# Kernel optimization log

Measured on AMD Instinct MI355X. Metric: run time of the kernel, lower is better.

## Reference

```python
import jax, jax.numpy as jnp
import numpy as np

# HashGrid config (from tcnn encoding config)
N_LEVELS = 16
N_FEATS = 2
LOG2_T = 19
T = 1 << LOG2_T  # 524288 entries per level
BASE_RES = 16
PER_LEVEL_SCALE = 1.5
PRIMES = (1, 2654435761, 805459861)  # tcnn spatial hash primes

# MLP config
N_NEURONS = 128
N_HIDDEN = 8  # 8 hidden layers -> w_in + 7 hidden matmuls + w_out
ENC_DIM = N_LEVELS * N_FEATS + 4  # 32 hashgrid feats + 4 identity dims
OUT_DIM = 3


def _level_params(level):
    # tcnn: scale = exp2(level*log2(s)) * base_res - 1 ; res = ceil(scale)+1
    scale = 2.0 ** (level * np.log2(PER_LEVEL_SCALE)) * BASE_RES - 1.0
    res = int(np.ceil(scale)) + 1
    return float(scale), res


def hash_grid_encode(x3, tables):
    """x3: [N,3] in [0,1]; tables: [L,T,F] -> [N, L*F]."""
    offs = jnp.array([[(c >> d) & 1 for d in range(3)] for c in range(8)], jnp.int32)  # [8,3]
    feats = []
    for l in range(N_LEVELS):
        scale, res = _level_params(l)
        pos = x3 * scale + 0.5
        p0 = jnp.floor(pos)
        frac = pos - p0                      # [N,3]
        p0 = p0.astype(jnp.int32)
        coords = p0[:, None, :] + offs[None, :, :]  # [N,8,3]
        # trilinear weights per corner
        w = jnp.where(offs[None, :, :] == 1, frac[:, None, :], 1.0 - frac[:, None, :]).prod(-1)  # [N,8]
        if res ** 3 <= T:
            # dense indexing (tcnn uses strided index while stride <= hashmap_size)
            idx = (coords[..., 0] + coords[..., 1] * res + coords[..., 2] * res * res) % T
        else:
            c = coords.astype(jnp.uint32)
            h = (c[..., 0] * jnp.uint32(PRIMES[0])
                 ^ c[..., 1] * jnp.uint32(PRIMES[1])
                 ^ c[..., 2] * jnp.uint32(PRIMES[2]))
            idx = (h & jnp.uint32(T - 1)).astype(jnp.int32)
        g = tables[l][idx]                   # [N,8,F] gather
        feats.append(jnp.einsum('nc,ncf->nf', w, g))  # [N,F]
    return jnp.concatenate(feats, axis=-1)   # [N,32]


def setup_inputs() -> dict:
    key = jax.random.key(0)
    kx, kt, k0, kh, ko = jax.random.split(key, 5)
    N = 524288
    x = jax.random.uniform(kx, (N, 16), dtype=jnp.float32)
    # tcnn hash tables init ~ U(-1e-4, 1e-4)
    tables = jax.random.uniform(kt, (N_LEVELS, T, N_FEATS), dtype=jnp.float32,
                                minval=-1e-4, maxval=1e-4)
    w_in = jax.random.normal(k0, (ENC_DIM, N_NEURONS), dtype=jnp.float32) * (1.0 / np.sqrt(ENC_DIM))
    w_hidden = jax.random.normal(kh, (N_HIDDEN - 1, N_NEURONS, N_NEURONS), dtype=jnp.float32) * (1.0 / np.sqrt(N_NEURONS))
    w_out = jax.random.normal(ko, (N_NEURONS, OUT_DIM), dtype=jnp.float32) * (1.0 / np.sqrt(N_NEURONS))
    return {"x": x, "tables": tables, "w_in": w_in, "w_hidden": w_hidden, "w_out": w_out}


def reference(x, tables, w_in, w_hidden, w_out):
    enc = jnp.concatenate([hash_grid_encode(x[:, :3], tables), x[:, 3:7]], axis=-1)  # [N,36]
    h = jax.nn.relu(enc @ w_in)
    for i in range(w_hidden.shape[0]):  # static small loop over 7 hidden layers
        h = jax.nn.relu(h @ w_hidden[i])
    return h @ w_out  # [N,3], linear output activation
```

## Files before the change

### kernel.cpp

```cpp
#include <hip/hip_runtime.h>
#include <math.h>

#define NPTS 524288
#define TSZ  524288
#define TMASK (TSZ - 1)

typedef _Float16 half8  __attribute__((ext_vector_type(8)));
typedef _Float16 half4v __attribute__((ext_vector_type(4)));
typedef float    f32x4  __attribute__((ext_vector_type(4)));

#define QSCALE    1.27e6f
#define ENC_SCALE 1024.f
#define DECF      (1e-4f / 127.f * ENC_SCALE)
#define WIN_SCALE (1.f / ENC_SCALE)

struct LevelParams {
  float    scale[16];
  int      res[16];
  unsigned dense_mask;
};

#define OFF_TAB 262144
#define OFF_XYZ 17039360
#define OFF_XID 25427968
#define OFF_ENC 29622272

__device__ __forceinline__ void convert_w_elem(int i,
    const float* __restrict__ w_in, const float* __restrict__ w_hidden,
    const float* __restrict__ w_out, _Float16* __restrict__ dst)
{
  float v;
  int dstidx;
  if (i < 8192) {
    int n = i >> 6, k = i & 63;
    if (k < 32) {
      int p = k >> 3, jj = (k >> 1) & 3, f = k & 1;
      int lev = (jj == 0) ? p : (4 + 3 * p + (jj - 1));
      v = w_in[(2 * lev + f) * 128 + n] * WIN_SCALE;
    } else if (k < 36) {
      v = w_in[k * 128 + n];
    } else v = 0.f;
    dstidx = n * 64 + (k ^ ((n & 7) << 3));
  } else if (i < 122880) {
    int r = i - 8192;
    int j = r >> 14, t = r & 16383;
    int n = t >> 7, k = t & 127;
    int q = ((k & 7) << 4) | (k >> 3);
    v = w_hidden[(j * 128 + q) * 128 + n];
    int h = k >> 6;
    dstidx = 8192 + j * 16384 + h * 8192 + n * 64 + ((k & 63) ^ ((n & 7) << 3));
  } else {
    int t = i - 122880;
    int n = t >> 7, k = t & 127;
    int q = ((k & 7) << 4) | (k >> 3);
    v = (n < 3) ? w_out[q * 3 + n] : 0.f;
    int h = k >> 6;
    dstidx = 122880 + h * 1024 + n * 64 + ((k & 63) ^ ((n & 7) << 3));
  }
  dst[dstidx] = (_Float16)v;
}

__global__ __launch_bounds__(256, 4)
void prep(const float* __restrict__ tables, const float* __restrict__ x,
          const float* __restrict__ w_in, const float* __restrict__ w_hidden,
          const float* __restrict__ w_out,
          unsigned* __restrict__ tab8w, f32x4* __restrict__ xyz,
          _Float16* __restrict__ xid, _Float16* __restrict__ wts)
{
  int i = blockIdx.x * 256 + threadIdx.x;
  if (i < 4194304) {
    f32x4 v = ((const f32x4*)tables)[i];
    int q0 = (int)rintf(v[0] * QSCALE);
    int q1 = (int)rintf(v[1] * QSCALE);
    int q2 = (int)rintf(v[2] * QSCALE);
    int q3 = (int)rintf(v[3] * QSCALE);
    tab8w[i] = (unsigned)(q0 & 255) | ((unsigned)(q1 & 255) << 8) |
               ((unsigned)(q2 & 255) << 16) | ((unsigned)(q3 & 255) << 24);
  } else if (i < 4718592) {
    int p = i - 4194304;
    f32x4 a = ((const f32x4*)x)[(size_t)p * 4];
    f32x4 b = ((const f32x4*)x)[(size_t)p * 4 + 1];
    xyz[p] = a;
    half4v h = {(_Float16)a[3], (_Float16)b[0], (_Float16)b[1], (_Float16)b[2]};
    *(half4v*)(xid + (size_t)p * 4) = h;
  } else {
    convert_w_elem(i - 4718592, w_in, w_hidden, w_out, wts);
  }
}

template<bool DENSE>
__device__ __forceinline__ void enc_one(float x0, float x1, float x2, float s,
    int res, unsigned rr, const unsigned short* __restrict__ tb,
    float& f0, float& f1)
{
  const float px = x0 * s + 0.5f, py = x1 * s + 0.5f, pz = x2 * s + 0.5f;
  const float fx = floorf(px), fy = floorf(py), fz = floorf(pz);
  const float wx1 = px - fx, wy1 = py - fy, wz1 = pz - fz;
  const float wx0 = 1.f - wx1, wy0 = 1.f - wy1, wz0 = 1.f - wz1;
  const unsigned ix = (unsigned)(int)fx, iy = (unsigned)(int)fy,
                 iz = (unsigned)(int)fz;
  unsigned t0, t1, u0, u1, v0, v1;
  if (DENSE) {
    t0 = ix; t1 = ix + 1u;
    u0 = iy * (unsigned)res; u1 = u0 + (unsigned)res;
    v0 = iz * rr; v1 = v0 + rr;
  } else {
    t0 = ix;               t1 = ix + 1u;
    u0 = iy * 2654435761u; u1 = (iy + 1u) * 2654435761u;
    v0 = iz * 805459861u;  v1 = (iz + 1u) * 805459861u;
  }
  f0 = 0.f; f1 = 0.f;
#pragma unroll
  for (int c = 0; c < 8; ++c) {
    const unsigned a = (c & 1) ? t1 : t0;
    const unsigned b = (c & 2) ? u1 : u0;
    const unsigned d = (c & 4) ? v1 : v0;
    const unsigned idx = DENSE ? (a + b + d) : ((a ^ b ^ d) & TMASK);
    const float w = ((c & 1) ? wx1 : wx0) * ((c & 2) ? wy1 : wy0) *
                    ((c & 4) ? wz1 : wz0);
    const unsigned g = tb[idx];
    f0 += w * (float)(int)(signed char)(g & 0xFFu);
    f1 += w * (float)(int)(signed char)(g >> 8);
  }
}

__global__ __launch_bounds__(256, 4)
void nrc_encode(const f32x4* __restrict__ xyz,
                const unsigned short* __restrict__ tab8,
                f32x4* __restrict__ enc16, LevelParams lp)
{
  const int bid = blockIdx.x;
  const int xcd = bid & 7;
  const int pr  = xcd >> 1;
  const int chunk = ((bid >> 3) << 1) | (xcd & 1);
  const float s0_ = lp.scale[pr];
  const int   res = lp.res[pr];
  const unsigned rr = (unsigned)(res * res);
  const float s1_ = lp.scale[4 + 3 * pr];
  const float s2_ = lp.scale[5 + 3 * pr];
  const float s3_ = lp.scale[6 + 3 * pr];
  const unsigned short* tb0 = tab8 + (size_t)pr * TSZ;
  const unsigned short* tb1 = tab8 + (size_t)(4 + 3 * pr) * TSZ;
  const unsigned short* tb2 = tab8 + (size_t)(5 + 3 * pr) * TSZ;
  const unsigned short* tb3 = tab8 + (size_t)(6 + 3 * pr) * TSZ;
  const int p0 = chunk * 1024 + threadIdx.x;

#pragma unroll 2
  for (int it = 0; it < 4; ++it) {
    const int pt = p0 + it * 256;
    const f32x4 xv = __builtin_nontemporal_load(xyz + pt);
    float f0, f1;
    half8 o;
    enc_one<true >(xv[0], xv[1], xv[2], s0_, res, rr, tb0, f0, f1);
    o[0] = (_Float16)(f0 * DECF); o[1] = (_Float16)(f1 * DECF);
    enc_one<false>(xv[0], xv[1], xv[2], s1_, 0, 0u, tb1, f0, f1);
    o[2] = (_Float16)(f0 * DECF); o[3] = (_Float16)(f1 * DECF);
    enc_one<false>(xv[0], xv[1], xv[2], s2_, 0, 0u, tb2, f0, f1);
    o[4] = (_Float16)(f0 * DECF); o[5] = (_Float16)(f1 * DECF);
    enc_one<false>(xv[0], xv[1], xv[2], s3_, 0, 0u, tb3, f0, f1);
    o[6] = (_Float16)(f0 * DECF); o[7] = (_Float16)(f1 * DECF);
    __builtin_nontemporal_store(*(const f32x4*)&o, enc16 + (size_t)pr * NPTS + pt);
  }
}

__device__ __forceinline__ void gload16(const void* g, void* l)
{
  __builtin_amdgcn_global_load_lds(
      (const __attribute__((address_space(1))) void*)g,
      (__attribute__((address_space(3))) void*)l, 16, 0, 0);
}

#define MFMA16 __builtin_amdgcn_mfma_f32_16x16x32_f16

#define STAGE(dst, srcoff, nch)                                   \
  for (int c = wave; c < (nch); c += 4)                           \
    gload16(wb + (srcoff) + c * 1024 + lane * 16, (dst) + c * 1024);

#define LOAD_A(hb)                                                \
  _Pragma("unroll")                                               \
  for (int t = 0; t < 4; ++t) {                                   \
    const char* At = A0 + t * 4096;                               \
    a0[t] = *(const half8*)(At + (((hb) + kg * 16) ^ s0));        \
    a1[t] = *(const half8*)(At + (((hb) + 64 + kg * 16) ^ s0));   \
  }

#define COMP_FRESH(WH)                                            \
  _Pragma("unroll")                                               \
  for (int n = 0; n < 8; ++n) {                                   \
    const int nr = n * 16 + c0;                                   \
    const char* Wr = (WH) + nr * 128;                             \
    const int wz = (nr & 7) << 4;                                 \
    half8 b0 = *(const half8*)(Wr + ((kg * 16) ^ wz));            \
    half8 b1 = *(const half8*)(Wr + ((64 + kg * 16) ^ wz));       \
    _Pragma("unroll")                                             \
    for (int t = 0; t < 4; ++t) {                                 \
      f32x4 z = {0.f, 0.f, 0.f, 0.f};                             \
      z = MFMA16(a0[t], b0, z, 0, 0, 0);                          \
      acc[t][n] = MFMA16(a1[t], b1, z, 0, 0, 0);                  \
    }                                                             \
  }

#define COMP_ACC(WH)                                              \
  _Pragma("unroll")                                               \
  for (int n = 0; n < 8; ++n) {                                   \
    const int nr = n * 16 + c0;                                   \
    const char* Wr = (WH) + nr * 128;                             \
    const int wz = (nr & 7) << 4;                                 \
    half8 b0 = *(const half8*)(Wr + ((kg * 16) ^ wz));            \
    half8 b1 = *(const half8*)(Wr + ((64 + kg * 16) ^ wz));       \
    _Pragma("unroll")                                             \
    for (int t = 0; t < 4; ++t) {                                 \
      acc[t][n] = MFMA16(a0[t], b0, acc[t][n], 0, 0, 0);          \
      acc[t][n] = MFMA16(a1[t], b1, acc[t][n], 0, 0, 0);          \
    }                                                             \
  }

#define RELU_WB                                                   \
  _Pragma("unroll")                                               \
  for (int t = 0; t < 4; ++t) {                                   \
    _Pragma("unroll")                                             \
    for (int r = 0; r < 4; ++r) {                                 \
      half8 v;                                                    \
      _Pragma("unroll")                                           \
      for (int n = 0; n < 8; ++n)                                 \
        v[n] = (_Float16)fmaxf(acc[t][n][r], 0.f);                \
      const int rw = dr0 + t * 16 + r;                            \
      *(half8*)(Xb + rw * 256 + ((c0 * 16) ^ ((rw & 7) << 4))) = v; \
    }                                                             \
  }

__global__ __launch_bounds__(256, 2)
void nrc_mlp(const f32x4* __restrict__ enc16, const _Float16* __restrict__ xid,
             const _Float16* __restrict__ wts, float* __restrict__ out)
{
  __shared__ __align__(16) char smem[98304];
  char* Xb  = smem;
  char* WH0 = smem + 65536;
  char* WH1 = smem + 81920;
  const char* wb = (const char*)wts;

  const int tid  = threadIdx.x;
  const int wave = tid >> 6;
  const int lane = tid & 63;
  const int blk  = blockIdx.x;

  STAGE(WH0, 0, 16);

  {
    const int gp = blk * 256 + tid;
    const int swz = (tid & 7) << 4;
    char* Xrow = Xb + tid * 256;
#pragma unroll
    for (int p = 0; p < 4; ++p) {
      f32x4 ef = enc16[(size_t)p * NPTS + gp];
      *(half8*)(Xrow + ((p * 16) ^ swz)) = *(half8*)&ef;
    }
    half8 z8;
#pragma unroll
    for (int i = 0; i < 8; ++i) z8[i] = (_Float16)0.f;
    const half4v iv = *(const half4v*)(xid + (size_t)gp * 4);
    half8 idv = z8;
    idv[0] = iv.x; idv[1] = iv.y; idv[2] = iv.z; idv[3] = iv.w;
    *(half8*)(Xrow + (64 ^ swz)) = idv;
    *(half8*)(Xrow + (80 ^ swz)) = z8;
    *(half8*)(Xrow + (96 ^ swz)) = z8;
    *(half8*)(Xrow + (112 ^ swz)) = z8;
  }
  __syncthreads();

  const int c0 = lane & 15;
  const int kg = lane >> 4;
  const int r0 = wave * 64 + c0;
  const int s0 = (r0 & 7) << 4;
  const char* A0 = Xb + (size_t)r0 * 256;
  const int dr0 = wave * 64 + kg * 4;

  f32x4 acc[4][8];
  half8 a0[4], a1[4];

  {
    STAGE(WH1, 16384, 16);
    LOAD_A(0);
    COMP_FRESH(WH0);
    RELU_WB;
  }
  __syncthreads();

#pragma unroll
  for (int j = 1; j <= 7; ++j) {
    {
      STAGE(WH0, 16384 + (j - 1) * 32768 + 16384, 16);
      LOAD_A(0);
      COMP_FRESH(WH1);
    }
    __syncthreads();
    {
      if (j < 7) {
        STAGE(WH1, 16384 + j * 32768, 16);
      } else {
        STAGE(WH1, 245760, 2);
      }
      LOAD_A(128);
      COMP_ACC(WH0);
      RELU_WB;
    }
    __syncthreads();
  }

  f32x4 zz[4];
  {
    STAGE(WH0, 247808, 2);
    LOAD_A(0);
    const char* Wr = WH1 + c0 * 128;
    const int wz = (c0 & 7) << 4;
    half8 b0 = *(const half8*)(Wr + ((kg * 16) ^ wz));
    half8 b1 = *(const half8*)(Wr + ((64 + kg * 16) ^ wz));
#pragma unroll
    for (int t = 0; t < 4; ++t) {
      f32x4 z = {0.f, 0.f, 0.f, 0.f};
      z = MFMA16(a0[t], b0, z, 0, 0, 0);
      zz[t] = MFMA16(a1[t], b1, z, 0, 0, 0);
    }
  }
  __syncthreads();
  {
    LOAD_A(128);
    const char* Wr = WH0 + c0 * 128;
    const int wz = (c0 & 7) << 4;
    half8 b0 = *(const half8*)(Wr + ((kg * 16) ^ wz));
    half8 b1 = *(const half8*)(Wr + ((64 + kg * 16) ^ wz));
#pragma unroll
    for (int t = 0; t < 4; ++t) {
      zz[t] = MFMA16(a0[t], b0, zz[t], 0, 0, 0);
      zz[t] = MFMA16(a1[t], b1, zz[t], 0, 0, 0);
    }
    if (c0 < 3) {
#pragma unroll
      for (int t = 0; t < 4; ++t) {
        const int pr0 = blk * 256 + dr0 + t * 16;
#pragma unroll
        for (int r = 0; r < 4; ++r)
          out[(size_t)(pr0 + r) * 3 + c0] = zz[t][r];
      }
    }
  }
}

extern "C" void kernel_launch(void* const* d_in, const int* in_sizes, int n_in,
                              void* d_out, int out_size, void* d_ws, size_t ws_size,
                              hipStream_t stream)
{
  const float* x        = (const float*)d_in[0];
  const float* tables   = (const float*)d_in[1];
  const float* w_in     = (const float*)d_in[2];
  const float* w_hidden = (const float*)d_in[3];
  const float* w_out    = (const float*)d_in[4];
  float* out = (float*)d_out;

  LevelParams lp;
  unsigned dm = 0;
  for (int l = 0; l < 16; ++l) {
    double scale = pow(2.0, (double)l * log2(1.5)) * 16.0 - 1.0;
    int res = (int)ceil(scale) + 1;
    lp.scale[l] = (float)scale;
    lp.res[l]   = res;
    if ((long long)res * res * res <= (long long)TSZ) dm |= (1u << l);
  }
  lp.dense_mask = dm;

  char* ws = (char*)d_ws;
  _Float16* wts   = (_Float16*)ws;
  unsigned* tab8w = (unsigned*)(ws + OFF_TAB);
  f32x4*    xyz   = (f32x4*)(ws + OFF_XYZ);
  _Float16* xid   = (_Float16*)(ws + OFF_XID);
  f32x4*    enc16 = (f32x4*)(ws + OFF_ENC);

  prep<<<18920, 256, 0, stream>>>(tables, x, w_in, w_hidden, w_out,
                                  tab8w, xyz, xid, wts);
  nrc_encode<<<2048, 256, 0, stream>>>(xyz, (const unsigned short*)tab8w,
                                       enc16, lp);
  nrc_mlp<<<2048, 256, 0, stream>>>(enc16, xid, wts, out);
}
```

Measured before the change: 533.3 us.

## Load MLP weights directly in MFMA fragment layout and batch hash-grid gathers

The weight prep now writes the fp16 weights pre-arranged in MFMA B-fragment order. This lets the MLP kernel read B operands straight from global memory, per lane, instead of staging them through LDS with block-wide barriers. Each wave now owns a private 16KB activation slice, so all __syncthreads are gone and LDS per block shrinks. The encode kernel computes all 32 gather indices before issuing the loads, which exposes more memory-level parallelism, and it halves points per block while doubling the grid. The cost is repeated global/L2 weight reads by every wave, plus higher register pressure in the encoder.

New measurement: 432.5 us. 1.23x faster.

```diff
diff --git a/kernel.cpp b/kernel.cpp
--- a/kernel.cpp
+++ b/kernel.cpp
@@ -25,39 +25,44 @@
 #define OFF_XID 25427968
 #define OFF_ENC 29622272
 
-__device__ __forceinline__ void convert_w_elem(int i,
+__device__ __forceinline__ _Float16 convert_w_val(int i,
     const float* __restrict__ w_in, const float* __restrict__ w_hidden,
-    const float* __restrict__ w_out, _Float16* __restrict__ dst)
-{
-  float v;
-  int dstidx;
+    const float* __restrict__ w_out)
+{
   if (i < 8192) {
-    int n = i >> 6, k = i & 63;
+    int b = i >> 9, r = i & 511;
+    int nt = b >> 1, s = b & 1;
+    int lane = r >> 3, e = r & 7;
+    int n = nt * 16 + (lane & 15);
+    int k = s * 32 + (lane >> 4) * 8 + e;
+    float v;
     if (k < 32) {
       int p = k >> 3, jj = (k >> 1) & 3, f = k & 1;
-      int lev = (jj == 0) ? p : (4 + 3 * p + (jj - 1));
+      int lev = jj ? (4 + 3 * p + jj - 1) : p;
       v = w_in[(2 * lev + f) * 128 + n] * WIN_SCALE;
     } else if (k < 36) {
       v = w_in[k * 128 + n];
     } else v = 0.f;
-    dstidx = n * 64 + (k ^ ((n & 7) << 3));
+    return (_Float16)v;
   } else if (i < 122880) {
-    int r = i - 8192;
-    int j = r >> 14, t = r & 16383;
-    int n = t >> 7, k = t & 127;
+    int t = i - 8192;
+    int j = t >> 14, u = t & 16383;
+    int b = u >> 9, r = u & 511;
+    int nt = b >> 2, s = b & 3;
+    int lane = r >> 3, e = r & 7;
+    int n = nt * 16 + (lane & 15);
+    int k = s * 32 + (lane >> 4) * 8 + e;
     int q = ((k & 7) << 4) | (k >> 3);
-    v = w_hidden[(j * 128 + q) * 128 + n];
-    int h = k >> 6;
-    dstidx = 8192 + j * 16384 + h * 8192 + n * 64 + ((k & 63) ^ ((n & 7) << 3));
+    return (_Float16)w_hidden[(j * 128 + q) * 128 + n];
   } else {
     int t = i - 122880;
-    int n = t >> 7, k = t & 127;
+    int s = t >> 9, r = t & 511;
+    int lane = r >> 3, e = r & 7;
+    int n = lane & 15;
+    int k = s * 32 + (lane >> 4) * 8 + e;
     int q = ((k & 7) << 4) | (k >> 3);
-    v = (n < 3) ? w_out[q * 3 + n] : 0.f;
-    int h = k >> 6;
-    dstidx = 122880 + h * 1024 + n * 64 + ((k & 63) ^ ((n & 7) << 3));
-  }
-  dst[dstidx] = (_Float16)v;
+    return (n < 3) ? (_Float16)w_out[q * 3 + n] : (_Float16)0.f;
+  }
 }
 
 __global__ __launch_bounds__(256, 4)
@@ -84,43 +89,7 @@
     half4v h = {(_Float16)a[3], (_Float16)b[0], (_Float16)b[1], (_Float16)b[2]};
     *(half4v*)(xid + (size_t)p * 4) = h;
   } else {
-    convert_w_elem(i - 4718592, w_in, w_hidden, w_out, wts);
-  }
-}
-
-template<bool DENSE>
-__device__ __forceinline__ void enc_one(float x0, float x1, float x2, float s,
-    int res, unsigned rr, const unsigned short* __restrict__ tb,
-    float& f0, float& f1)
-{
-  const float px = x0 * s + 0.5f, py = x1 * s + 0.5f, pz = x2 * s + 0.5f;
-  const float fx = floorf(px), fy = floorf(py), fz = floorf(pz);
-  const float wx1 = px - fx, wy1 = py - fy, wz1 = pz - fz;
-  const float wx0 = 1.f - wx1, wy0 = 1.f - wy1, wz0 = 1.f - wz1;
-  const unsigned ix = (unsigned)(int)fx, iy = (unsigned)(int)fy,
-                 iz = (unsigned)(int)fz;
-  unsigned t0, t1, u0, u1, v0, v1;
-  if (DENSE) {
-    t0 = ix; t1 = ix + 1u;
-    u0 = iy * (unsigned)res; u1 = u0 + (unsigned)res;
-    v0 = iz * rr; v1 = v0 + rr;
-  } else {
-    t0 = ix;               t1 = ix + 1u;
-    u0 = iy * 2654435761u; u1 = (iy + 1u) * 2654435761u;
-    v0 = iz * 805459861u;  v1 = (iz + 1u) * 805459861u;
-  }
-  f0 = 0.f; f1 = 0.f;
-#pragma unroll
-  for (int c = 0; c < 8; ++c) {
-    const unsigned a = (c & 1) ? t1 : t0;
-    const unsigned b = (c & 2) ? u1 : u0;
-    const unsigned d = (c & 4) ? v1 : v0;
-    const unsigned idx = DENSE ? (a + b + d) : ((a ^ b ^ d) & TMASK);
-    const float w = ((c & 1) ? wx1 : wx0) * ((c & 2) ? wy1 : wy0) *
-                    ((c & 4) ? wz1 : wz0);
-    const unsigned g = tb[idx];
-    f0 += w * (float)(int)(signed char)(g & 0xFFu);
-    f1 += w * (float)(int)(signed char)(g >> 8);
+    wts[i - 4718592] = convert_w_val(i - 4718592, w_in, w_hidden, w_out);
   }
 }
 
@@ -133,123 +102,99 @@
   const int xcd = bid & 7;
   const int pr  = xcd >> 1;
   const int chunk = ((bid >> 3) << 1) | (xcd & 1);
-  const float s0_ = lp.scale[pr];
-  const int   res = lp.res[pr];
+  const float sc0 = lp.scale[pr];
+  const float sc1 = lp.scale[4 + 3 * pr];
+  const float sc2 = lp.scale[5 + 3 * pr];
+  const float sc3 = lp.scale[6 + 3 * pr];
+  const int res = lp.res[pr];
   const unsigned rr = (unsigned)(res * res);
-  const float s1_ = lp.scale[4 + 3 * pr];
-  const float s2_ = lp.scale[5 + 3 * pr];
-  const float s3_ = lp.scale[6 + 3 * pr];
   const unsigned short* tb0 = tab8 + (size_t)pr * TSZ;
   const unsigned short* tb1 = tab8 + (size_t)(4 + 3 * pr) * TSZ;
   const unsigned short* tb2 = tab8 + (size_t)(5 + 3 * pr) * TSZ;
   const unsigned short* tb3 = tab8 + (size_t)(6 + 3 * pr) * TSZ;
-  const int p0 = chunk * 1024 + threadIdx.x;
-
-#pragma unroll 2
-  for (int it = 0; it < 4; ++it) {
+  const int p0 = chunk * 512 + threadIdx.x;
+
+#pragma unroll
+  for (int it = 0; it < 2; ++it) {
     const int pt = p0 + it * 256;
     const f32x4 xv = __builtin_nontemporal_load(xyz + pt);
-    float f0, f1;
+    float wxa[4], wya[4], wza[4];
+    unsigned idxs[4][8];
+#pragma unroll
+    for (int l = 0; l < 4; ++l) {
+      const float s = (l == 0) ? sc0 : (l == 1) ? sc1 : (l == 2) ? sc2 : sc3;
+      const float px = xv[0] * s + 0.5f, py = xv[1] * s + 0.5f,
+                  pz = xv[2] * s + 0.5f;
+      const float fx = floorf(px), fy = floorf(py), fz = floorf(pz);
+      wxa[l] = px - fx; wya[l] = py - fy; wza[l] = pz - fz;
+      const unsigned ix = (unsigned)(int)fx, iy = (unsigned)(int)fy,
+                     iz = (unsigned)(int)fz;
+      unsigned t0, t1, u0, u1, v0, v1;
+      if (l == 0) {
+        t0 = ix; t1 = ix + 1u;
+        u0 = iy * (unsigned)res; u1 = u0 + (unsigned)res;
+        v0 = iz * rr; v1 = v0 + rr;
+      } else {
+        t0 = ix;               t1 = ix + 1u;
+        u0 = iy * 2654435761u; u1 = (iy + 1u) * 2654435761u;
+        v0 = iz * 805459861u;  v1 = (iz + 1u) * 805459861u;
+      }
+#pragma unroll
+      for (int c = 0; c < 8; ++c) {
+        const unsigned a = (c & 1) ? t1 : t0;
+        const unsigned b = (c & 2) ? u1 : u0;
+        const unsigned d = (c & 4) ? v1 : v0;
+        idxs[l][c] = (l == 0) ? (a + b + d) : ((a ^ b ^ d) & TMASK);
+      }
+    }
+    unsigned gv[4][8];
+#pragma unroll
+    for (int c = 0; c < 8; ++c) gv[0][c] = tb0[idxs[0][c]];
+#pragma unroll
+    for (int c = 0; c < 8; ++c) gv[1][c] = tb1[idxs[1][c]];
+#pragma unroll
+    for (int c = 0; c < 8; ++c) gv[2][c] = tb2[idxs[2][c]];
+#pragma unroll
+    for (int c = 0; c < 8; ++c) gv[3][c] = tb3[idxs[3][c]];
     half8 o;
-    enc_one<true >(xv[0], xv[1], xv[2], s0_, res, rr, tb0, f0, f1);
-    o[0] = (_Float16)(f0 * DECF); o[1] = (_Float16)(f1 * DECF);
-    enc_one<false>(xv[0], xv[1], xv[2], s1_, 0, 0u, tb1, f0, f1);
-    o[2] = (_Float16)(f0 * DECF); o[3] = (_Float16)(f1 * DECF);
-    enc_one<false>(xv[0], xv[1], xv[2], s2_, 0, 0u, tb2, f0, f1);
-    o[4] = (_Float16)(f0 * DECF); o[5] = (_Float16)(f1 * DECF);
-    enc_one<false>(xv[0], xv[1], xv[2], s3_, 0, 0u, tb3, f0, f1);
-    o[6] = (_Float16)(f0 * DECF); o[7] = (_Float16)(f1 * DECF);
-    __builtin_nontemporal_store(*(const f32x4*)&o, enc16 + (size_t)pr * NPTS + pt);
-  }
-}
-
-__device__ __forceinline__ void gload16(const void* g, void* l)
-{
-  __builtin_amdgcn_global_load_lds(
-      (const __attribute__((address_space(1))) void*)g,
-      (__attribute__((address_space(3))) void*)l, 16, 0, 0);
+#pragma unroll
+    for (int l = 0; l < 4; ++l) {
+      const float wx1 = wxa[l], wy1 = wya[l], wz1 = wza[l];
+      const float wx0 = 1.f - wx1, wy0 = 1.f - wy1, wz0 = 1.f - wz1;
+      float f0 = 0.f, f1 = 0.f;
+#pragma unroll
+      for (int c = 0; c < 8; ++c) {
+        const float w = ((c & 1) ? wx1 : wx0) * ((c & 2) ? wy1 : wy0) *
+                        ((c & 4) ? wz1 : wz0);
+        f0 += w * (float)(int)(signed char)(gv[l][c] & 255u);
+        f1 += w * (float)(int)(signed char)(gv[l][c] >> 8);
+      }
+      o[2 * l]     = (_Float16)(f0 * DECF);
+      o[2 * l + 1] = (_Float16)(f1 * DECF);
+    }
+    __builtin_nontemporal_store(*(const f32x4*)&o,
+                                enc16 + (size_t)pr * NPTS + pt);
+  }
 }
 
 #define MFMA16 __builtin_amdgcn_mfma_f32_16x16x32_f16
-
-#define STAGE(dst, srcoff, nch)                                   \
-  for (int c = wave; c < (nch); c += 4)                           \
-    gload16(wb + (srcoff) + c * 1024 + lane * 16, (dst) + c * 1024);
-
-#define LOAD_A(hb)                                                \
-  _Pragma("unroll")                                               \
-  for (int t = 0; t < 4; ++t) {                                   \
-    const char* At = A0 + t * 4096;                               \
-    a0[t] = *(const half8*)(At + (((hb) + kg * 16) ^ s0));        \
-    a1[t] = *(const half8*)(At + (((hb) + 64 + kg * 16) ^ s0));   \
-  }
-
-#define COMP_FRESH(WH)                                            \
-  _Pragma("unroll")                                               \
-  for (int n = 0; n < 8; ++n) {                                   \
-    const int nr = n * 16 + c0;                                   \
-    const char* Wr = (WH) + nr * 128;                             \
-    const int wz = (nr & 7) << 4;                                 \
-    half8 b0 = *(const half8*)(Wr + ((kg * 16) ^ wz));            \
-    half8 b1 = *(const half8*)(Wr + ((64 + kg * 16) ^ wz));       \
-    _Pragma("unroll")                                             \
-    for (int t = 0; t < 4; ++t) {                                 \
-      f32x4 z = {0.f, 0.f, 0.f, 0.f};                             \
-      z = MFMA16(a0[t], b0, z, 0, 0, 0);                          \
-      acc[t][n] = MFMA16(a1[t], b1, z, 0, 0, 0);                  \
-    }                                                             \
-  }
-
-#define COMP_ACC(WH)                                              \
-  _Pragma("unroll")                                               \
-  for (int n = 0; n < 8; ++n) {                                   \
-    const int nr = n * 16 + c0;                                   \
-    const char* Wr = (WH) + nr * 128;                             \
-    const int wz = (nr & 7) << 4;                                 \
-    half8 b0 = *(const half8*)(Wr + ((kg * 16) ^ wz));            \
-    half8 b1 = *(const half8*)(Wr + ((64 + kg * 16) ^ wz));       \
-    _Pragma("unroll")                                             \
-    for (int t = 0; t < 4; ++t) {                                 \
-      acc[t][n] = MFMA16(a0[t], b0, acc[t][n], 0, 0, 0);          \
-      acc[t][n] = MFMA16(a1[t], b1, acc[t][n], 0, 0, 0);          \
-    }                                                             \
-  }
-
-#define RELU_WB                                                   \
-  _Pragma("unroll")                                               \
-  for (int t = 0; t < 4; ++t) {                                   \
-    _Pragma("unroll")                                             \
-    for (int r = 0; r < 4; ++r) {                                 \
-      half8 v;                                                    \
-      _Pragma("unroll")                                           \
-      for (int n = 0; n < 8; ++n)                                 \
-        v[n] = (_Float16)fmaxf(acc[t][n][r], 0.f);                \
-      const int rw = dr0 + t * 16 + r;                            \
-      *(half8*)(Xb + rw * 256 + ((c0 * 16) ^ ((rw & 7) << 4))) = v; \
-    }                                                             \
-  }
 
 __global__ __launch_bounds__(256, 2)
 void nrc_mlp(const f32x4* __restrict__ enc16, const _Float16* __restrict__ xid,
              const _Float16* __restrict__ wts, float* __restrict__ out)
 {
-  __shared__ __align__(16) char smem[98304];
-  char* Xb  = smem;
-  char* WH0 = smem + 65536;
-  char* WH1 = smem + 81920;
-  const char* wb = (const char*)wts;
-
+  __shared__ __align__(16) char smem[65536];
   const int tid  = threadIdx.x;
   const int wave = tid >> 6;
   const int lane = tid & 63;
   const int blk  = blockIdx.x;
-
-  STAGE(WH0, 0, 16);
+  char* Xw = smem + (wave << 14);
+  const char* wb = (const char*)wts;
 
   {
-    const int gp = blk * 256 + tid;
-    const int swz = (tid & 7) << 4;
-    char* Xrow = Xb + tid * 256;
+    const int gp = blk * 256 + wave * 64 + lane;
+    const int swz = (lane & 7) << 4;
+    char* Xrow = Xw + lane * 256;
 #pragma unroll
     for (int p = 0; p < 4; ++p) {
       f32x4 ef = enc16[(size_t)p * NPTS + gp];
@@ -261,83 +206,111 @@
     const half4v iv = *(const half4v*)(xid + (size_t)gp * 4);
     half8 idv = z8;
     idv[0] = iv.x; idv[1] = iv.y; idv[2] = iv.z; idv[3] = iv.w;
-    *(half8*)(Xrow + (64 ^ swz)) = idv;
-    *(half8*)(Xrow + (80 ^ swz)) = z8;
-    *(half8*)(Xrow + (96 ^ swz)) = z8;
+    *(half8*)(Xrow + (64 ^ swz))  = idv;
+    *(half8*)(Xrow + (80 ^ swz))  = z8;
+    *(half8*)(Xrow + (96 ^ swz))  = z8;
     *(half8*)(Xrow + (112 ^ swz)) = z8;
   }
-  __syncthreads();
 
   const int c0 = lane & 15;
   const int kg = lane >> 4;
-  const int r0 = wave * 64 + c0;
-  const int s0 = (r0 & 7) << 4;
-  const char* A0 = Xb + (size_t)r0 * 256;
-  const int dr0 = wave * 64 + kg * 4;
+  const char* A0 = Xw + c0 * 256;
+  const int s0 = (c0 & 7) << 4;
+  const int dr0 = kg * 4;
 
   f32x4 acc[4][8];
-  half8 a0[4], a1[4];
 
   {
-    STAGE(WH1, 16384, 16);
-    LOAD_A(0);
-    COMP_FRESH(WH0);
-    RELU_WB;
-  }
-  __syncthreads();
-
-#pragma unroll
+    half8 a0[4], a1[4];
+#pragma unroll
+    for (int t = 0; t < 4; ++t) {
+      a0[t] = *(const half8*)(A0 + t * 4096 + ((kg * 16) ^ s0));
+      a1[t] = *(const half8*)(A0 + t * 4096 + ((64 + kg * 16) ^ s0));
+    }
+#pragma unroll
+    for (int n = 0; n < 8; ++n) {
+      half8 b0 = *(const half8*)(wb + (n * 2) * 1024 + lane * 16);
+      half8 b1 = *(const half8*)(wb + (n * 2 + 1) * 1024 + lane * 16);
+#pragma unroll
+      for (int t = 0; t < 4; ++t) {
+        f32x4 z = {0.f, 0.f, 0.f, 0.f};
+        z = MFMA16(a0[t], b0, z, 0, 0, 0);
+        acc[t][n] = MFMA16(a1[t], b1, z, 0, 0, 0);
+      }
+    }
+#pragma unroll
+    for (int t = 0; t < 4; ++t)
+#pragma unroll
+      for (int r = 0; r < 4; ++r) {
+        half8 v;
+#pragma unroll
+        for (int n = 0; n < 8; ++n) v[n] = (_Float16)fmaxf(acc[t][n][r], 0.f);
+        const int rw = dr0 + t * 16 + r;
+        *(half8*)(Xw + rw * 256 + ((c0 * 16) ^ ((rw & 7) << 4))) = v;
+      }
+  }
+
+#pragma unroll 1
   for (int j = 1; j <= 7; ++j) {
-    {
-      STAGE(WH0, 16384 + (j - 1) * 32768 + 16384, 16);
-      LOAD_A(0);
-      COMP_FRESH(WH1);
-    }
-    __syncthreads();
-    {
-      if (j < 7) {
-        STAGE(WH1, 16384 + j * 32768, 16);
-      } else {
-        STAGE(WH1, 245760, 2);
-      }
-      LOAD_A(128);
-      COMP_ACC(WH0);
-      RELU_WB;
-    }
-    __syncthreads();
-  }
-
-  f32x4 zz[4];
+    const char* wj = wb + 16384 + (j - 1) * 32768;
+#pragma unroll
+    for (int s = 0; s < 4; ++s) {
+      half8 a[4];
+#pragma unroll
+      for (int t = 0; t < 4; ++t)
+        a[t] = *(const half8*)(A0 + t * 4096 + ((s * 64 + kg * 16) ^ s0));
+      half8 b[8];
+#pragma unroll
+      for (int n = 0; n < 8; ++n)
+        b[n] = *(const half8*)(wj + (n * 4 + s) * 1024 + lane * 16);
+#pragma unroll
+      for (int n = 0; n < 8; ++n)
+#pragma unroll
+        for (int t = 0; t < 4; ++t) {
+          if (s == 0) {
+            f32x4 z = {0.f, 0.f, 0.f, 0.f};
+            acc[t][n] = MFMA16(a[t], b[n], z, 0, 0, 0);
+          } else {
+            acc[t][n] = MFMA16(a[t], b[n], acc[t][n], 0, 0, 0);
+          }
+        }
+    }
+#pragma unroll
+    for (int t = 0; t < 4; ++t)
+#pragma unroll
+      for (int r = 0; r < 4; ++r) {
+        half8 v;
+#pragma unroll
+        for (int n = 0; n < 8; ++n) v[n] = (_Float16)fmaxf(acc[t][n][r], 0.f);
+        const int rw = dr0 + t * 16 + r;
+        *(half8*)(Xw + rw * 256 + ((c0 * 16) ^ ((rw & 7) << 4))) = v;
+      }
+  }
+
   {
-    STAGE(WH0, 247808, 2);
-    LOAD_A(0);
-    const char* Wr = WH1 + c0 * 128;
-    const int wz = (c0 & 7) << 4;
-    half8 b0 = *(const half8*)(Wr + ((kg * 16) ^ wz));
-    half8 b1 = *(const half8*)(Wr + ((64 + kg * 16) ^ wz));
-#pragma unroll
-    for (int t = 0; t < 4; ++t) {
-      f32x4 z = {0.f, 0.f, 0.f, 0.f};
-      z = MFMA16(a0[t], b0, z, 0, 0, 0);
-      zz[t] = MFMA16(a1[t], b1, z, 0, 0, 0);
-    }
-  }
-  __syncthreads();
-  {
-    LOAD_A(128);
-    const char* Wr = WH0 + c0 * 128;
-    const int wz = (c0 & 7) << 4;
-    half8 b0 = *(const half8*)(Wr + ((kg * 16) ^ wz));
-    half8 b1 = *(const half8*)(Wr + ((64 + kg * 16) ^ wz));
-#pragma unroll
-    for (int t = 0; t < 4; ++t) {
-      zz[t] = MFMA16(a0[t], b0, zz[t], 0, 0, 0);
-      zz[t] = MFMA16(a1[t], b1, zz[t], 0, 0, 0);
+    const char* w8 = wb + 245760;
+    f32x4 zz[4];
+#pragma unroll
+    for (int s = 0; s < 4; ++s) {
+      half8 a[4];
+#pragma unroll
+      for (int t = 0; t < 4; ++t)
+        a[t] = *(const half8*)(A0 + t * 4096 + ((s * 64 + kg * 16) ^ s0));
+      half8 b = *(const half8*)(w8 + s * 1024 + lane * 16);
+#pragma unroll
+      for (int t = 0; t < 4; ++t) {
+        if (s == 0) {
+          f32x4 z = {0.f, 0.f, 0.f, 0.f};
+          zz[t] = MFMA16(a[t], b, z, 0, 0, 0);
+        } else {
+          zz[t] = MFMA16(a[t], b, zz[t], 0, 0, 0);
+        }
+      }
     }
     if (c0 < 3) {
 #pragma unroll
       for (int t = 0; t < 4; ++t) {
-        const int pr0 = blk * 256 + dr0 + t * 16;
+        const int pr0 = blk * 256 + wave * 64 + t * 16 + dr0;
 #pragma unroll
         for (int r = 0; r < 4; ++r)
           out[(size_t)(pr0 + r) * 3 + c0] = zz[t][r];
@@ -377,7 +350,7 @@
 
   prep<<<18920, 256, 0, stream>>>(tables, x, w_in, w_hidden, w_out,
                                   tab8w, xyz, xid, wts);
-  nrc_encode<<<2048, 256, 0, stream>>>(xyz, (const unsigned short*)tab8w,
+  nrc_encode<<<4096, 256, 0, stream>>>(xyz, (const unsigned short*)tab8w,
                                        enc16, lp);
   nrc_mlp<<<2048, 256, 0, stream>>>(enc16, xid, wts, out);
 }
```
